# Optimization experiments

Measured on AMD Instinct MI355X. Metric: run time of the kernel, lower is better.

The kernel has to match this reference:

```python
import jax, jax.numpy as jnp
import numpy as np

S, H, W = 32, 64, 64
WS = (4, 4, 4)
SH = (2, 2, 2)  # shift = window//2
C, NH = 192, 6
N = WS[0] * WS[1] * WS[2]  # 64 tokens per window
HD = C // NH
NWIN = (S // WS[0]) * (H // WS[1]) * (W // WS[2])


def _rel_pos_index():
    c = np.stack(np.meshgrid(*[np.arange(w) for w in WS], indexing='ij')).reshape(3, -1)
    r = (c[:, :, None] - c[:, None, :]).transpose(1, 2, 0)
    r[..., 0] += WS[0] - 1; r[..., 1] += WS[1] - 1; r[..., 2] += WS[2] - 1
    r[..., 0] *= (2 * WS[1] - 1) * (2 * WS[2] - 1)
    r[..., 1] *= (2 * WS[2] - 1)
    return r.sum(-1)  # (N, N)


def _attn_mask():
    m = np.zeros((S, H, W))
    cnt = 0
    sl = lambda w, s: (slice(0, -w), slice(-w, -s), slice(-s, None))
    for ss in sl(WS[0], SH[0]):
        for hs in sl(WS[1], SH[1]):
            for ws_ in sl(WS[2], SH[2]):
                m[ss, hs, ws_] = cnt; cnt += 1
    mw = m.reshape(S // WS[0], WS[0], H // WS[1], WS[1], W // WS[2], WS[2])
    mw = mw.transpose(0, 2, 4, 1, 3, 5).reshape(-1, N)
    am = mw[:, None, :] - mw[:, :, None]
    return np.where(am != 0, -100.0, 0.0).astype(np.float32)  # (nW, N, N)


RPI = _rel_pos_index()
AMASK = _attn_mask()


def ln(x, g, b):
    mu = x.mean(-1, keepdims=True)
    v = ((x - mu) ** 2).mean(-1, keepdims=True)
    return (x - mu) / jnp.sqrt(v + 1e-5) * g + b


def win_part(x):  # (B,S,H,W,C) -> (B*nW, N, C)
    B = x.shape[0]
    x = x.reshape(B, S // WS[0], WS[0], H // WS[1], WS[1], W // WS[2], WS[2], C)
    return x.transpose(0, 1, 3, 5, 2, 4, 6, 7).reshape(-1, N, C)


def win_rev(w, B):  # (B*nW, N, C) -> (B,S,H,W,C)
    x = w.reshape(B, S // WS[0], H // WS[1], W // WS[2], WS[0], WS[1], WS[2], C)
    return x.transpose(0, 1, 4, 2, 5, 3, 6, 7).reshape(B, S, H, W, C)


def block(x, g1, b1, qw, qb, rpb, pw, pb, g2, b2, f1w, f1b, f2w, f2b, shifted):
    B, L, _ = x.shape
    shortcut = x
    h = ln(x, g1, b1).reshape(B, S, H, W, C)
    if shifted:
        h = jnp.roll(h, (-SH[0], -SH[1], -SH[2]), (1, 2, 3))
    xw = win_part(h)                                     # (Bn, N, C)
    Bn = xw.shape[0]
    qkv = (xw @ qw + qb).reshape(Bn, N, 3, NH, HD).transpose(2, 0, 3, 1, 4)
    q, k, v = qkv[0] * (HD ** -0.5), qkv[1], qkv[2]
    attn = jnp.einsum('bhnd,bhmd->bhnm', q, k)           # (Bn, NH, N, N)
    bias = rpb[RPI.reshape(-1)].reshape(N, N, NH).transpose(2, 0, 1)
    attn = attn + bias[None]
    if shifted:
        attn = attn.reshape(B, NWIN, NH, N, N) + jnp.asarray(AMASK)[None, :, None]
        attn = attn.reshape(Bn, NH, N, N)
    attn = jax.nn.softmax(attn, axis=-1)
    o = jnp.einsum('bhnm,bhmd->bhnd', attn, v).transpose(0, 2, 1, 3).reshape(Bn, N, C)
    o = o @ pw + pb
    h = win_rev(o, B)
    if shifted:
        h = jnp.roll(h, SH, (1, 2, 3))
    x = shortcut + h.reshape(B, L, C)
    h = ln(x, g2, b2)
    h = jax.nn.gelu(h @ f1w + f1b, approximate=False) @ f2w + f2b
    return x + h


def setup_inputs() -> dict:
    key = jax.random.key(0)
    ks = iter(jax.random.split(key, 32))
    d = {'x': jax.random.normal(next(ks), (1, S * H * W, C), jnp.float32)}
    for s in ('0', '1'):
        d['g1_' + s] = jnp.ones((C,), jnp.float32)
        d['b1_' + s] = jnp.zeros((C,), jnp.float32)
        d['qw_' + s] = 0.02 * jax.random.normal(next(ks), (C, 3 * C), jnp.float32)
        d['qb_' + s] = jnp.zeros((3 * C,), jnp.float32)
        d['rpb_' + s] = 0.02 * jax.random.normal(next(ks), (343, NH), jnp.float32)
        d['pw_' + s] = 0.02 * jax.random.normal(next(ks), (C, C), jnp.float32)
        d['pb_' + s] = jnp.zeros((C,), jnp.float32)
        d['g2_' + s] = jnp.ones((C,), jnp.float32)
        d['b2_' + s] = jnp.zeros((C,), jnp.float32)
        d['f1w_' + s] = 0.02 * jax.random.normal(next(ks), (C, 4 * C), jnp.float32)
        d['f1b_' + s] = jnp.zeros((4 * C,), jnp.float32)
        d['f2w_' + s] = 0.02 * jax.random.normal(next(ks), (4 * C, C), jnp.float32)
        d['f2b_' + s] = jnp.zeros((C,), jnp.float32)
    return d


def reference(x, g1_0, b1_0, qw_0, qb_0, rpb_0, pw_0, pb_0, g2_0, b2_0, f1w_0, f1b_0, f2w_0, f2b_0,
              g1_1, b1_1, qw_1, qb_1, rpb_1, pw_1, pb_1, g2_1, b2_1, f1w_1, f1b_1, f2w_1, f2b_1):
    x = block(x, g1_0, b1_0, qw_0, qb_0, rpb_0, pw_0, pb_0, g2_0, b2_0, f1w_0, f1b_0, f2w_0, f2b_0, False)
    x = block(x, g1_1, b1_1, qw_1, qb_1, rpb_1, pw_1, pb_1, g2_1, b2_1, f1w_1, f1b_1, f2w_1, f2b_1, True)
    return x
```

## Files before the change

### kernel.cpp

```cpp
#include <hip/hip_runtime.h>
#include <math.h>


#define L_TOK 131072
#define C_DIM 192
#define NWIN 2048

typedef unsigned int uint32;
typedef unsigned short u16;
typedef __bf16 bf16x8 __attribute__((ext_vector_type(8)));
typedef __bf16 bf16x4 __attribute__((ext_vector_type(4)));
typedef float f32x4 __attribute__((ext_vector_type(4)));

__device__ __forceinline__ u16 f2bf(float f) {
    uint32 u = __float_as_uint(f);
    u += 0x7fffu + ((u >> 16) & 1u);
    return (u16)(u >> 16);
}
__device__ __forceinline__ float bf2f(u16 h) { return __uint_as_float(((uint32)h) << 16); }

__device__ __forceinline__ float gelu_f(float x) {
    const float x2 = x * x;
    const float inner = x * fmaf(0.044715f, x2, 1.0f);
    const float e = __expf(-1.5957691216057308f * inner);
    return x * __builtin_amdgcn_rcpf(1.0f + e);
}

__device__ __forceinline__ int win_row_to_token(int r, int shifted) {
    const int win = r >> 6, n = r & 63;
    const int sb = win >> 8, hb = (win >> 4) & 15, wb = win & 15;
    int gz = sb * 4 + (n >> 4);
    int gy = hb * 4 + ((n >> 2) & 3);
    int gx = wb * 4 + (n & 3);
    if (shifted) { gz = (gz + 2) & 31; gy = (gy + 2) & 63; gx = (gx + 2) & 63; }
    return (gz << 12) | (gy << 6) | gx;
}

__device__ __forceinline__ void gll16(const u16* g, u16* l) {
    __builtin_amdgcn_global_load_lds((const __attribute__((address_space(1))) void*)g,
                                     (__attribute__((address_space(3))) void*)l, 16, 0, 0);
}

__device__ __forceinline__ void stage_wchunk4(const u16* __restrict__ gsrc, u16* lds) {
    const int wave = threadIdx.x >> 6, lane = threadIdx.x & 63;
    for (int c = wave; c < 25; c += 4)
        gll16(gsrc + c * 512 + lane * 8, lds + c * 512);
}

__device__ __forceinline__ void stage_wchunk8(const u16* __restrict__ gsrc, u16* lds) {
    const int wave = threadIdx.x >> 6, lane = threadIdx.x & 63;
    for (int c = wave; c < 27; c += 8)
        gll16(gsrc + c * 512 + lane * 8, lds + c * 512);
}

__device__ __forceinline__ void stage_hchunk8(const u16* __restrict__ gsrc, u16* lds) {
    const int wave = threadIdx.x >> 6, lane = threadIdx.x & 63;
    for (int c = wave; c < 36; c += 8)
        gll16(gsrc + c * 512 + lane * 8, lds + c * 512);
}

struct WtSeg { const float* in; u16* out; int N; int nelem; int mode; };
struct WtTable { WtSeg s[8]; };

__global__ __launch_bounds__(256) void wtrans_all_kernel(WtTable t) {
    int idx = blockIdx.x * 256 + threadIdx.x;
#pragma unroll
    for (int si = 0; si < 8; ++si) {
        const WtSeg& sg = t.s[si];
        if (idx < sg.nelem) {
            if (sg.mode == 0) {
                const int n = idx / 192, k = idx - n * 192;
                sg.out[n * 200 + k] = f2bf(sg.in[(size_t)k * sg.N + n]);
            } else {
                const int n = idx / 768, k = idx - n * 768;
                sg.out[(k >> 6) * 13824 + n * 72 + (k & 63)] = f2bf(sg.in[(size_t)k * 192 + n]);
            }
            return;
        }
        idx -= sg.nelem;
    }
}

__global__ __launch_bounds__(256) void rpbt_kernel(const float* __restrict__ r0,
                                                   const float* __restrict__ r1,
                                                   float* __restrict__ o0,
                                                   float* __restrict__ o1) {
    const int idx = blockIdx.x * 256 + threadIdx.x;
    if (idx < 343 * 6) {
        const int h = idx / 343, r = idx - h * 343;
        o0[idx] = r0[r * 6 + h];
        o1[idx] = r1[r * 6 + h];
    }
}

__device__ __forceinline__ void load_tok_regs(const u16* __restrict__ base, bf16x8 (&xb)[2][6]) {
    const int lane = threadIdx.x & 63, wave = threadIdx.x >> 6;
    const int i = lane & 15, g = lane >> 4;
#pragma unroll
    for (int tt = 0; tt < 2; ++tt)
#pragma unroll
        for (int ks = 0; ks < 6; ++ks)
            xb[tt][ks] = *(const bf16x8*)(base + (size_t)(32 * wave + 16 * tt + i) * 192 +
                                          32 * ks + 8 * g);
}

__global__ __launch_bounds__(256) void qkv_ln_mfma(const float* __restrict__ X,
                                                   const float* __restrict__ g1,
                                                   const float* __restrict__ b1,
                                                   const u16* __restrict__ qwT,
                                                   const float* __restrict__ qb,
                                                   u16* __restrict__ q, u16* __restrict__ k,
                                                   u16* __restrict__ v, int shifted) {
    __shared__ __align__(16) u16 Bs[2][64 * 200];
    const int m0 = blockIdx.x * 128;
    const int lane = threadIdx.x & 63, wave = threadIdx.x >> 6;
    const int i = lane & 15, g = lane >> 4;

    stage_wchunk4(qwT, Bs[0]);

    bf16x8 xb[2][6];
#pragma unroll
    for (int tt = 0; tt < 2; ++tt) {
        const int m = m0 + 32 * wave + 16 * tt + i;
        const int t = win_row_to_token(m, shifted);
        const float* xr = X + (size_t)t * C_DIM;
        float vv[6][8];
        float s = 0.0f;
#pragma unroll
        for (int ks = 0; ks < 6; ++ks) {
            const float4 a = *(const float4*)(xr + 32 * ks + 8 * g);
            const float4 b = *(const float4*)(xr + 32 * ks + 8 * g + 4);
            vv[ks][0] = a.x; vv[ks][1] = a.y; vv[ks][2] = a.z; vv[ks][3] = a.w;
            vv[ks][4] = b.x; vv[ks][5] = b.y; vv[ks][6] = b.z; vv[ks][7] = b.w;
            s += a.x + a.y + a.z + a.w + b.x + b.y + b.z + b.w;
        }
        s += __shfl_xor(s, 16, 64);
        s += __shfl_xor(s, 32, 64);
        const float mu = s * (1.0f / 192.0f);
        float sq = 0.0f;
#pragma unroll
        for (int ks = 0; ks < 6; ++ks)
#pragma unroll
            for (int j = 0; j < 8; ++j) {
                const float d = vv[ks][j] - mu;
                sq += d * d;
            }
        sq += __shfl_xor(sq, 16, 64);
        sq += __shfl_xor(sq, 32, 64);
        const float rstd = rsqrtf(sq * (1.0f / 192.0f) + 1e-5f);
#pragma unroll
        for (int ks = 0; ks < 6; ++ks) {
            const int c0 = 32 * ks + 8 * g;
            const float4 ga = *(const float4*)(g1 + c0);
            const float4 gb = *(const float4*)(g1 + c0 + 4);
            const float4 ba = *(const float4*)(b1 + c0);
            const float4 bb = *(const float4*)(b1 + c0 + 4);
            u16 tmp[8];
            tmp[0] = f2bf((vv[ks][0] - mu) * rstd * ga.x + ba.x);
            tmp[1] = f2bf((vv[ks][1] - mu) * rstd * ga.y + ba.y);
            tmp[2] = f2bf((vv[ks][2] - mu) * rstd * ga.z + ba.z);
            tmp[3] = f2bf((vv[ks][3] - mu) * rstd * ga.w + ba.w);
            tmp[4] = f2bf((vv[ks][4] - mu) * rstd * gb.x + bb.x);
            tmp[5] = f2bf((vv[ks][5] - mu) * rstd * gb.y + bb.y);
            tmp[6] = f2bf((vv[ks][6] - mu) * rstd * gb.z + bb.z);
            tmp[7] = f2bf((vv[ks][7] - mu) * rstd * gb.w + bb.w);
            xb[tt][ks] = *(const bf16x8*)tmp;
        }
    }

    __syncthreads();
#pragma unroll 1
    for (int nc = 0; nc < 9; ++nc) {
        const int cur = nc & 1;
        if (nc < 8) stage_wchunk4(qwT + (size_t)(nc + 1) * 12800, Bs[cur ^ 1]);
        f32x4 acc[4][2] = {};
        const u16* paw = Bs[cur] + i * 200 + 8 * g;
#pragma unroll
        for (int ks = 0; ks < 6; ++ks) {
#pragma unroll
            for (int a = 0; a < 4; ++a) {
                const bf16x8 av = *(const bf16x8*)(paw + a * 16 * 200 + ks * 32);
                acc[a][0] = __builtin_amdgcn_mfma_f32_16x16x32_bf16(av, xb[0][ks], acc[a][0], 0, 0, 0);
                acc[a][1] = __builtin_amdgcn_mfma_f32_16x16x32_bf16(av, xb[1][ks], acc[a][1], 0, 0, 0);
            }
        }
        const int which = nc / 3;
        u16* dst = (which == 0) ? q : (which == 1) ? k : v;
        const float sc = (which == 0) ? 0.17677669529663687f : 1.0f;
#pragma unroll
        for (int a = 0; a < 4; ++a) {
            const int n0 = nc * 64 + 16 * a + 4 * g;
            const int hn = n0 - which * 192;
            const int head = hn >> 5, hd0 = hn & 31;
            const float4 bi = *(const float4*)(qb + n0);
#pragma unroll
            for (int tt = 0; tt < 2; ++tt) {
                const int m = m0 + wave * 32 + 16 * tt + i;
                const int win = m >> 6, tok = m & 63;
                ushort4 pk;
                pk.x = f2bf((acc[a][tt][0] + bi.x) * sc);
                pk.y = f2bf((acc[a][tt][1] + bi.y) * sc);
                pk.z = f2bf((acc[a][tt][2] + bi.z) * sc);
                pk.w = f2bf((acc[a][tt][3] + bi.w) * sc);
                *(ushort4*)(dst + ((size_t)(win * 6 + head) * 64 + tok) * 32 + hd0) = pk;
            }
        }
        __syncthreads();
    }
}

__global__ __launch_bounds__(256) void attn_mfma(const u16* __restrict__ qg,
                                                 const u16* __restrict__ kg,
                                                 const u16* __restrict__ vg,
                                                 const float* __restrict__ rpbT,
                                                 u16* __restrict__ o, int shifted) {
    __shared__ __align__(16) u16 vt[32 * 68];
    __shared__ __align__(16) u16 ps[64 * 68];
    __shared__ __align__(16) u16 os[64 * 40];
    __shared__ float bias_s[343];
    __shared__ int ms[64];
    const int tid = threadIdx.x;
    const int lane = tid & 63, w = tid >> 6;
    const int i = lane & 15, g = lane >> 4;
    const int head = blockIdx.x >> 11;
    const int win = blockIdx.x & 2047;
    const size_t base = (size_t)(win * 6 + head) * 2048;

    const bf16x8 qf = *(const bf16x8*)(qg + base + (size_t)(16 * w + i) * 32 + 8 * g);
    bf16x8 kf[4];
#pragma unroll
    for (int t = 0; t < 4; ++t)
        kf[t] = *(const bf16x8*)(kg + base + (size_t)(16 * t + i) * 32 + 8 * g);
    {
        const int n = tid >> 2, c0 = (tid & 3) * 8;
        uint4 raw = *(const uint4*)(vg + base + (size_t)n * 32 + c0);
        const u16* pr = (const u16*)&raw;
#pragma unroll
        for (int j = 0; j < 8; ++j) vt[(c0 + j) * 68 + n] = pr[j];
    }
    for (int idx = tid; idx < 343; idx += 256) bias_s[idx] = rpbT[head * 343 + idx];
    if (tid < 64) {
        int mv = 0;
        if (shifted) {
            const int sb = win >> 8, hb = (win >> 4) & 15, wb = win & 15;
            const int gz = sb * 4 + (tid >> 4);
            const int gy = hb * 4 + ((tid >> 2) & 3);
            const int gx = wb * 4 + (tid & 3);
            const int rz = gz < 28 ? 0 : (gz < 30 ? 1 : 2);
            const int ry = gy < 60 ? 0 : (gy < 62 ? 1 : 2);
            const int rw = gx < 60 ? 0 : (gx < 62 ? 1 : 2);
            mv = rz * 9 + ry * 3 + rw;
        }
        ms[tid] = mv;
    }
    __syncthreads();

    __builtin_amdgcn_s_setprio(1);
    const f32x4 zero = {0.0f, 0.0f, 0.0f, 0.0f};
    f32x4 s[4];
#pragma unroll
    for (int t = 0; t < 4; ++t)
        s[t] = __builtin_amdgcn_mfma_f32_16x16x32_bf16(kf[t], qf, zero, 0, 0, 0);

    const int qrow = 16 * w + i;
    const int mq = ms[qrow];
    float p[16];
#pragma unroll
    for (int t = 0; t < 4; ++t)
#pragma unroll
        for (int r = 0; r < 4; ++r) {
            const int j = 16 * t + 4 * g + r;
            const int dz = (qrow >> 4) - (j >> 4) + 3;
            const int dy = ((qrow >> 2) & 3) - ((j >> 2) & 3) + 3;
            const int dx = (qrow & 3) - (j & 3) + 3;
            float val = s[t][r] + bias_s[dz * 49 + dy * 7 + dx];
            if (shifted && (mq != ms[j])) val -= 100.0f;
            p[t * 4 + r] = val;
        }
    float mx = -3.0e38f;
#pragma unroll
    for (int u = 0; u < 16; ++u) mx = fmaxf(mx, p[u]);
    mx = fmaxf(mx, __shfl_xor(mx, 16, 64));
    mx = fmaxf(mx, __shfl_xor(mx, 32, 64));
    float sum = 0.0f;
#pragma unroll
    for (int u = 0; u < 16; ++u) { p[u] = __expf(p[u] - mx); sum += p[u]; }
    sum += __shfl_xor(sum, 16, 64);
    sum += __shfl_xor(sum, 32, 64);
    const float inv = __builtin_amdgcn_rcpf(sum);

#pragma unroll
    for (int t = 0; t < 4; ++t) {
        ushort4 pk;
        pk.x = f2bf(p[t * 4 + 0] * inv); pk.y = f2bf(p[t * 4 + 1] * inv);
        pk.z = f2bf(p[t * 4 + 2] * inv); pk.w = f2bf(p[t * 4 + 3] * inv);
        *(ushort4*)(ps + (size_t)qrow * 68 + 16 * t + 4 * g) = pk;
    }

    f32x4 oacc[2] = {zero, zero};
#pragma unroll
    for (int kb = 0; kb < 2; ++kb) {
        const bf16x4 alo = *(const bf16x4*)(ps + (size_t)qrow * 68 + 8 * g + 32 * kb);
        const bf16x4 ahi = *(const bf16x4*)(ps + (size_t)qrow * 68 + 8 * g + 32 * kb + 4);
        const bf16x8 a = __builtin_shufflevector(alo, ahi, 0, 1, 2, 3, 4, 5, 6, 7);
#pragma unroll
        for (int ct = 0; ct < 2; ++ct) {
            const bf16x4 blo = *(const bf16x4*)(vt + (size_t)(i + 16 * ct) * 68 + 8 * g + 32 * kb);
            const bf16x4 bhi = *(const bf16x4*)(vt + (size_t)(i + 16 * ct) * 68 + 8 * g + 32 * kb + 4);
            const bf16x8 b = __builtin_shufflevector(blo, bhi, 0, 1, 2, 3, 4, 5, 6, 7);
            oacc[ct] = __builtin_amdgcn_mfma_f32_16x16x32_bf16(a, b, oacc[ct], 0, 0, 0);
        }
    }
    __builtin_amdgcn_s_setprio(0);
#pragma unroll
    for (int ct = 0; ct < 2; ++ct)
#pragma unroll
        for (int r = 0; r < 4; ++r)
            os[(16 * w + 4 * g + r) * 40 + i + 16 * ct] = f2bf(oacc[ct][r]);
    __syncthreads();
    {
        const int n = tid >> 2, c0 = (tid & 3) * 8;
        const uint4 val = *(const uint4*)(os + n * 40 + c0);
        *(uint4*)(o + (size_t)(win * 64 + n) * C_DIM + head * 32 + c0) = val;
    }
}

__global__ __launch_bounds__(256) void proj_ln_mfma(const u16* __restrict__ o,
                                                    const u16* __restrict__ pwT,
                                                    const float* __restrict__ pb,
                                                    const float* xin,
                                                    const float* __restrict__ g2,
                                                    const float* __restrict__ b2,
                                                    float* x2, u16* __restrict__ x2n,
                                                    int shifted) {
    __shared__ __align__(16) u16 Bs[2][64 * 200];
    const int m0 = blockIdx.x * 128;
    const int lane = threadIdx.x & 63, wave = threadIdx.x >> 6;
    const int i = lane & 15, g = lane >> 4;
    stage_wchunk4(pwT, Bs[0]);
    bf16x8 xb[2][6];
    load_tok_regs(o + (size_t)m0 * 192, xb);
    __syncthreads();
    f32x4 acc[12][2] = {};
#pragma unroll
    for (int nc = 0; nc < 3; ++nc) {
        const int cur = nc & 1;
        if (nc < 2) stage_wchunk4(pwT + (size_t)(nc + 1) * 12800, Bs[cur ^ 1]);
        const u16* paw = Bs[cur] + i * 200 + 8 * g;
#pragma unroll
        for (int ks = 0; ks < 6; ++ks) {
#pragma unroll
            for (int a = 0; a < 4; ++a) {
                const bf16x8 av = *(const bf16x8*)(paw + a * 16 * 200 + ks * 32);
                acc[nc * 4 + a][0] = __builtin_amdgcn_mfma_f32_16x16x32_bf16(av, xb[0][ks], acc[nc * 4 + a][0], 0, 0, 0);
                acc[nc * 4 + a][1] = __builtin_amdgcn_mfma_f32_16x16x32_bf16(av, xb[1][ks], acc[nc * 4 + a][1], 0, 0, 0);
            }
        }
        __syncthreads();
    }
#pragma unroll
    for (int tt = 0; tt < 2; ++tt) {
        const int m = m0 + wave * 32 + 16 * tt + i;
        const int t = win_row_to_token(m, shifted);
        const float* xr = xin + (size_t)t * C_DIM;
        float s = 0.0f;
#pragma unroll
        for (int a = 0; a < 12; ++a) {
            const int n0 = 16 * a + 4 * g;
            const float4 xv = *(const float4*)(xr + n0);
            const float4 bi = *(const float4*)(pb + n0);
            acc[a][tt][0] += xv.x + bi.x;
            acc[a][tt][1] += xv.y + bi.y;
            acc[a][tt][2] += xv.z + bi.z;
            acc[a][tt][3] += xv.w + bi.w;
            s += acc[a][tt][0] + acc[a][tt][1] + acc[a][tt][2] + acc[a][tt][3];
        }
        s += __shfl_xor(s, 16, 64);
        s += __shfl_xor(s, 32, 64);
        const float mu = s * (1.0f / 192.0f);
        float sq = 0.0f;
#pragma unroll
        for (int a = 0; a < 12; ++a) {
#pragma unroll
            for (int r = 0; r < 4; ++r) {
                const float d = acc[a][tt][r] - mu;
                sq += d * d;
            }
        }
        sq += __shfl_xor(sq, 16, 64);
        sq += __shfl_xor(sq, 32, 64);
        const float rstd = rsqrtf(sq * (1.0f / 192.0f) + 1e-5f);
        float* x2r = x2 + (size_t)t * C_DIM;
        u16* xnr = x2n + (size_t)t * C_DIM;
#pragma unroll
        for (int a = 0; a < 12; ++a) {
            const int n0 = 16 * a + 4 * g;
            float4 wv;
            wv.x = acc[a][tt][0]; wv.y = acc[a][tt][1];
            wv.z = acc[a][tt][2]; wv.w = acc[a][tt][3];
            *(float4*)(x2r + n0) = wv;
            const float4 gv = *(const float4*)(g2 + n0);
            const float4 bv = *(const float4*)(b2 + n0);
            ushort4 nk;
            nk.x = f2bf((wv.x - mu) * rstd * gv.x + bv.x);
            nk.y = f2bf((wv.y - mu) * rstd * gv.y + bv.y);
            nk.z = f2bf((wv.z - mu) * rstd * gv.z + bv.z);
            nk.w = f2bf((wv.w - mu) * rstd * gv.w + bv.w);
            *(ushort4*)(xnr + n0) = nk;
        }
    }
}

__global__ __launch_bounds__(256) void fc1_mfma(const u16* __restrict__ x2n,
                                                const u16* __restrict__ f1wT,
                                                const float* __restrict__ f1b,
                                                u16* __restrict__ h_t) {
    __shared__ __align__(16) u16 Bs[2][64 * 200];
    const int m0 = blockIdx.x * 128;
    const int lane = threadIdx.x & 63, wave = threadIdx.x >> 6;
    const int i = lane & 15, g = lane >> 4;
    stage_wchunk4(f1wT, Bs[0]);
    bf16x8 xb[2][6];
    load_tok_regs(x2n + (size_t)m0 * 192, xb);
    __syncthreads();
#pragma unroll 1
    for (int nc = 0; nc < 12; ++nc) {
        const int cur = nc & 1;
        if (nc < 11) stage_wchunk4(f1wT + (size_t)(nc + 1) * 12800, Bs[cur ^ 1]);
        f32x4 acc[4][2] = {};
        const u16* paw = Bs[cur] + i * 200 + 8 * g;
#pragma unroll
        for (int ks = 0; ks < 6; ++ks) {
#pragma unroll
            for (int a = 0; a < 4; ++a) {
                const bf16x8 av = *(const bf16x8*)(paw + a * 16 * 200 + ks * 32);
                acc[a][0] = __builtin_amdgcn_mfma_f32_16x16x32_bf16(av, xb[0][ks], acc[a][0], 0, 0, 0);
                acc[a][1] = __builtin_amdgcn_mfma_f32_16x16x32_bf16(av, xb[1][ks], acc[a][1], 0, 0, 0);
            }
        }
        u16* hchunk = h_t + (size_t)nc * ((size_t)L_TOK * 72);
#pragma unroll
        for (int a = 0; a < 4; ++a) {
            const int c0 = 16 * a + 4 * g;
            const float4 bi = *(const float4*)(f1b + nc * 64 + c0);
#pragma unroll
            for (int tt = 0; tt < 2; ++tt) {
                const int m = m0 + wave * 32 + 16 * tt + i;
                ushort4 pk;
                pk.x = f2bf(gelu_f(acc[a][tt][0] + bi.x));
                pk.y = f2bf(gelu_f(acc[a][tt][1] + bi.y));
                pk.z = f2bf(gelu_f(acc[a][tt][2] + bi.z));
                pk.w = f2bf(gelu_f(acc[a][tt][3] + bi.w));
                *(ushort4*)(hchunk + (size_t)m * 72 + c0) = pk;
            }
        }
        __syncthreads();
    }
}

__global__ __launch_bounds__(512) void fc2_mfma(const u16* __restrict__ h_t,
                                                const u16* __restrict__ f2wT,
                                                const float* __restrict__ f2b,
                                                const float* x2, float* out) {
    __shared__ __align__(16) u16 As[256 * 72];
    __shared__ __align__(16) u16 Bs[192 * 72];
    const int tid = threadIdx.x, lane = tid & 63, wave = tid >> 6;
    const int i = lane & 15, g = lane >> 4;
    const int m0 = blockIdx.x * 256;
    f32x4 acc[12][2] = {};
#pragma unroll 1
    for (int kc = 0; kc < 12; ++kc) {
        stage_hchunk8(h_t + (size_t)kc * ((size_t)L_TOK * 72) + (size_t)m0 * 72, As);
        stage_wchunk8(f2wT + (size_t)kc * 13824, Bs);
        __syncthreads();
        const u16* pbt = As + (wave * 32 + i) * 72 + 8 * g;
        const u16* paw = Bs + i * 72 + 8 * g;
#pragma unroll
        for (int ks = 0; ks < 2; ++ks) {
            const bf16x8 b0 = *(const bf16x8*)(pbt + ks * 32);
            const bf16x8 b1 = *(const bf16x8*)(pbt + 16 * 72 + ks * 32);
#pragma unroll
            for (int a = 0; a < 12; ++a) {
                const bf16x8 av = *(const bf16x8*)(paw + a * 16 * 72 + ks * 32);
                acc[a][0] = __builtin_amdgcn_mfma_f32_16x16x32_bf16(av, b0, acc[a][0], 0, 0, 0);
                acc[a][1] = __builtin_amdgcn_mfma_f32_16x16x32_bf16(av, b1, acc[a][1], 0, 0, 0);
            }
        }
        __syncthreads();
    }
#pragma unroll
    for (int tt = 0; tt < 2; ++tt) {
        const int m = m0 + wave * 32 + 16 * tt + i;
        const float* x2r = x2 + (size_t)m * C_DIM;
        float* orow = out + (size_t)m * C_DIM;
#pragma unroll
        for (int a = 0; a < 12; ++a) {
            const int n0 = 16 * a + 4 * g;
            const float4 xv = *(const float4*)(x2r + n0);
            const float4 bi = *(const float4*)(f2b + n0);
            float4 rr;
            rr.x = xv.x + bi.x + acc[a][tt][0];
            rr.y = xv.y + bi.y + acc[a][tt][1];
            rr.z = xv.z + bi.z + acc[a][tt][2];
            rr.w = xv.w + bi.w + acc[a][tt][3];
            *(float4*)(orow + n0) = rr;
        }
    }
}

static void run_block(const float* X, float* XOUT,
                      const float* g1, const float* b1, const float* qb,
                      const float* rpbT, const float* pb,
                      const float* g2, const float* b2,
                      const float* f1b, const float* f2b,
                      const u16* qwT, const u16* pwT, const u16* f1wT, const u16* f2wT,
                      int shifted, char* ws, hipStream_t stream) {
    const size_t PB = (size_t)L_TOK * C_DIM * sizeof(u16);
    u16* o   = (u16*)ws;
    u16* q   = (u16*)(ws + PB);
    u16* k   = (u16*)(ws + 2 * PB);
    u16* v   = (u16*)(ws + 3 * PB);
    u16* h_t = (u16*)(ws + PB);
    u16* x2n = (u16*)(ws + 6 * PB);
    float* x2 = XOUT;

    qkv_ln_mfma<<<L_TOK / 128, 256, 0, stream>>>(X, g1, b1, qwT, qb, q, k, v, shifted);
    attn_mfma<<<NWIN * 6, 256, 0, stream>>>(q, k, v, rpbT, o, shifted);
    proj_ln_mfma<<<L_TOK / 128, 256, 0, stream>>>(o, pwT, pb, X, g2, b2, x2, x2n, shifted);
    fc1_mfma<<<L_TOK / 128, 256, 0, stream>>>(x2n, f1wT, f1b, h_t);
    fc2_mfma<<<L_TOK / 256, 512, 0, stream>>>(h_t, f2wT, f2b, x2, XOUT);
}

extern "C" void kernel_launch(void* const* d_in, const int* in_sizes, int n_in,
                              void* d_out, int out_size, void* d_ws, size_t ws_size,
                              hipStream_t stream) {
    const float* x = (const float*)d_in[0];
    float* out = (float*)d_out;
    char* ws = (char*)d_ws;
    auto in = [&](int i) { return (const float*)d_in[i]; };

    const size_t offW = (size_t)L_TOK * C_DIM * sizeof(u16) * 7;
    u16* wbase = (u16*)(ws + offW);
    const size_t SQ = 115200, SP = 38400, SF1 = 153600, SF2 = 165888;
    const size_t WBLK = SQ + SP + SF1 + SF2;
    u16* qwT[2]  = { wbase,                    wbase + WBLK };
    u16* pwT[2]  = { wbase + SQ,               wbase + WBLK + SQ };
    u16* f1wT[2] = { wbase + SQ + SP,          wbase + WBLK + SQ + SP };
    u16* f2wT[2] = { wbase + SQ + SP + SF1,    wbase + WBLK + SQ + SP + SF1 };
    float* rpbT0 = (float*)(wbase + 2 * WBLK);
    float* rpbT1 = rpbT0 + 6 * 343;

    WtTable wt;
    wt.s[0] = { in(3),  qwT[0],  576, 576 * 192, 0 };
    wt.s[1] = { in(6),  pwT[0],  192, 192 * 192, 0 };
    wt.s[2] = { in(10), f1wT[0], 768, 768 * 192, 0 };
    wt.s[3] = { in(12), f2wT[0], 192, 192 * 768, 1 };
    wt.s[4] = { in(16), qwT[1],  576, 576 * 192, 0 };
    wt.s[5] = { in(19), pwT[1],  192, 192 * 192, 0 };
    wt.s[6] = { in(23), f1wT[1], 768, 768 * 192, 0 };
    wt.s[7] = { in(25), f2wT[1], 192, 192 * 768, 1 };
    int total = 0;
    for (int s = 0; s < 8; ++s) total += wt.s[s].nelem;
    wtrans_all_kernel<<<(total + 255) / 256, 256, 0, stream>>>(wt);
    rpbt_kernel<<<(343 * 6 + 255) / 256, 256, 0, stream>>>(in(5), in(18), rpbT0, rpbT1);

    run_block(x, out, in(1), in(2), in(4), rpbT0, in(7), in(8), in(9), in(11), in(13),
              qwT[0], pwT[0], f1wT[0], f2wT[0], 0, ws, stream);
    run_block(out, out, in(14), in(15), in(17), rpbT1, in(20), in(21), in(22), in(24), in(26),
              qwT[1], pwT[1], f1wT[1], f2wT[1], 1, ws, stream);
}
```

Before: 793.1 us.

## Store FC1 output and FC2 weights in MFMA fragment order, drop fc2 LDS staging

The fc1 epilogue now writes the hidden activations in a layout that matches the MFMA operand fragments fc2 consumes, and the fc2 weight transpose emits the same pre-swizzled fragment order. fc2 then loads both operands straight from global memory into registers with contiguous 16-byte loads, with no LDS staging and no block barriers. This removes the LDS round trip and the syncs, at the cost of every wave reading the weight fragments directly from global/L2 and leaving no explicit prefetch of the next k-chunk.

```diff
diff --git a/kernel.cpp b/kernel.cpp
--- a/kernel.cpp
+++ b/kernel.cpp
@@ -47,18 +47,6 @@
         gll16(gsrc + c * 512 + lane * 8, lds + c * 512);
 }
 
-__device__ __forceinline__ void stage_wchunk8(const u16* __restrict__ gsrc, u16* lds) {
-    const int wave = threadIdx.x >> 6, lane = threadIdx.x & 63;
-    for (int c = wave; c < 27; c += 8)
-        gll16(gsrc + c * 512 + lane * 8, lds + c * 512);
-}
-
-__device__ __forceinline__ void stage_hchunk8(const u16* __restrict__ gsrc, u16* lds) {
-    const int wave = threadIdx.x >> 6, lane = threadIdx.x & 63;
-    for (int c = wave; c < 36; c += 8)
-        gll16(gsrc + c * 512 + lane * 8, lds + c * 512);
-}
-
 struct WtSeg { const float* in; u16* out; int N; int nelem; int mode; };
 struct WtTable { WtSeg s[8]; };
 
@@ -73,7 +61,12 @@
                 sg.out[n * 200 + k] = f2bf(sg.in[(size_t)k * sg.N + n]);
             } else {
                 const int n = idx / 768, k = idx - n * 768;
-                sg.out[(k >> 6) * 13824 + n * 72 + (k & 63)] = f2bf(sg.in[(size_t)k * 192 + n]);
+                const int kc = k >> 6, ck = k & 63;
+                const int ks = ck >> 5, gq = (ck >> 3) & 3, j = ck & 7;
+                const int a = n >> 4, i = n & 15;
+                const size_t off =
+                    ((((size_t)kc * 12 + a) * 2 + ks) * 64 + (gq * 16 + i)) * 8 + j;
+                sg.out[off] = f2bf(sg.in[(size_t)k * 192 + n]);
             }
             return;
         }
@@ -414,7 +407,7 @@
 __global__ __launch_bounds__(256) void fc1_mfma(const u16* __restrict__ x2n,
                                                 const u16* __restrict__ f1wT,
                                                 const float* __restrict__ f1b,
-                                                u16* __restrict__ h_t) {
+                                                u16* __restrict__ h2) {
     __shared__ __align__(16) u16 Bs[2][64 * 200];
     const int m0 = blockIdx.x * 128;
     const int lane = threadIdx.x & 63, wave = threadIdx.x >> 6;
@@ -423,6 +416,8 @@
     bf16x8 xb[2][6];
     load_tok_regs(x2n + (size_t)m0 * 192, xb);
     __syncthreads();
+    const int blk2 = blockIdx.x >> 1;
+    const int wave2 = ((blockIdx.x & 1) << 2) | wave;
 #pragma unroll 1
     for (int nc = 0; nc < 12; ++nc) {
         const int cur = nc & 1;
@@ -438,55 +433,54 @@
                 acc[a][1] = __builtin_amdgcn_mfma_f32_16x16x32_bf16(av, xb[1][ks], acc[a][1], 0, 0, 0);
             }
         }
-        u16* hchunk = h_t + (size_t)nc * ((size_t)L_TOK * 72);
+        u16* hch = h2 + (size_t)nc * 8388608 + (size_t)blk2 * 16384;
 #pragma unroll
         for (int a = 0; a < 4; ++a) {
             const int c0 = 16 * a + 4 * g;
+            const int ksx = a >> 1;
+            const int g2 = (2 * a + (g >> 1)) & 3;
+            const int j0 = (g & 1) * 4;
             const float4 bi = *(const float4*)(f1b + nc * 64 + c0);
 #pragma unroll
             for (int tt = 0; tt < 2; ++tt) {
-                const int m = m0 + wave * 32 + 16 * tt + i;
+                const int tid2 = wave2 * 64 + g2 * 16 + i;
                 ushort4 pk;
                 pk.x = f2bf(gelu_f(acc[a][tt][0] + bi.x));
                 pk.y = f2bf(gelu_f(acc[a][tt][1] + bi.y));
                 pk.z = f2bf(gelu_f(acc[a][tt][2] + bi.z));
                 pk.w = f2bf(gelu_f(acc[a][tt][3] + bi.w));
-                *(ushort4*)(hchunk + (size_t)m * 72 + c0) = pk;
+                *(ushort4*)(hch + (size_t)(ksx * 2 + tt) * 4096 + tid2 * 8 + j0) = pk;
             }
         }
         __syncthreads();
     }
 }
 
-__global__ __launch_bounds__(512) void fc2_mfma(const u16* __restrict__ h_t,
+__global__ __launch_bounds__(512) void fc2_mfma(const u16* __restrict__ h2,
                                                 const u16* __restrict__ f2wT,
                                                 const float* __restrict__ f2b,
                                                 const float* x2, float* out) {
-    __shared__ __align__(16) u16 As[256 * 72];
-    __shared__ __align__(16) u16 Bs[192 * 72];
     const int tid = threadIdx.x, lane = tid & 63, wave = tid >> 6;
     const int i = lane & 15, g = lane >> 4;
     const int m0 = blockIdx.x * 256;
     f32x4 acc[12][2] = {};
 #pragma unroll 1
     for (int kc = 0; kc < 12; ++kc) {
-        stage_hchunk8(h_t + (size_t)kc * ((size_t)L_TOK * 72) + (size_t)m0 * 72, As);
-        stage_wchunk8(f2wT + (size_t)kc * 13824, Bs);
-        __syncthreads();
-        const u16* pbt = As + (wave * 32 + i) * 72 + 8 * g;
-        const u16* paw = Bs + i * 72 + 8 * g;
+        const u16* ab = h2 + (size_t)kc * 8388608 + (size_t)blockIdx.x * 16384 + tid * 8;
+        bf16x8 af[4];
+#pragma unroll
+        for (int fr = 0; fr < 4; ++fr)
+            af[fr] = *(const bf16x8*)(ab + fr * 4096);
+        const u16* wb = f2wT + (size_t)kc * 12288 + lane * 8;
 #pragma unroll
         for (int ks = 0; ks < 2; ++ks) {
-            const bf16x8 b0 = *(const bf16x8*)(pbt + ks * 32);
-            const bf16x8 b1 = *(const bf16x8*)(pbt + 16 * 72 + ks * 32);
 #pragma unroll
             for (int a = 0; a < 12; ++a) {
-                const bf16x8 av = *(const bf16x8*)(paw + a * 16 * 72 + ks * 32);
-                acc[a][0] = __builtin_amdgcn_mfma_f32_16x16x32_bf16(av, b0, acc[a][0], 0, 0, 0);
-                acc[a][1] = __builtin_amdgcn_mfma_f32_16x16x32_bf16(av, b1, acc[a][1], 0, 0, 0);
-            }
-        }
-        __syncthreads();
+                const bf16x8 av = *(const bf16x8*)(wb + a * 1024 + ks * 512);
+                acc[a][0] = __builtin_amdgcn_mfma_f32_16x16x32_bf16(av, af[ks * 2 + 0], acc[a][0], 0, 0, 0);
+                acc[a][1] = __builtin_amdgcn_mfma_f32_16x16x32_bf16(av, af[ks * 2 + 1], acc[a][1], 0, 0, 0);
+            }
+        }
     }
 #pragma unroll
     for (int tt = 0; tt < 2; ++tt) {
@@ -520,15 +514,15 @@
     u16* q   = (u16*)(ws + PB);
     u16* k   = (u16*)(ws + 2 * PB);
     u16* v   = (u16*)(ws + 3 * PB);
-    u16* h_t = (u16*)(ws + PB);
+    u16* h2  = (u16*)(ws + PB);
     u16* x2n = (u16*)(ws + 6 * PB);
     float* x2 = XOUT;
 
     qkv_ln_mfma<<<L_TOK / 128, 256, 0, stream>>>(X, g1, b1, qwT, qb, q, k, v, shifted);
     attn_mfma<<<NWIN * 6, 256, 0, stream>>>(q, k, v, rpbT, o, shifted);
     proj_ln_mfma<<<L_TOK / 128, 256, 0, stream>>>(o, pwT, pb, X, g2, b2, x2, x2n, shifted);
-    fc1_mfma<<<L_TOK / 128, 256, 0, stream>>>(x2n, f1wT, f1b, h_t);
-    fc2_mfma<<<L_TOK / 256, 512, 0, stream>>>(h_t, f2wT, f2b, x2, XOUT);
+    fc1_mfma<<<L_TOK / 128, 256, 0, stream>>>(x2n, f1wT, f1b, h2);
+    fc2_mfma<<<L_TOK / 256, 512, 0, stream>>>(h2, f2wT, f2b, x2, XOUT);
 }
 
 extern "C" void kernel_launch(void* const* d_in, const int* in_sizes, int n_in,
```

Result: slower. 870.4 us (+9.7%).
